# Performance work log

Measured on AMD Instinct MI355X. Metric: run time of the kernel, lower is better.

## Reference

```python
import jax, jax.numpy as jnp
import numpy as np

IDIM = 512
HDIM = 1024
CDIM = 128  # part_size; topk uses k = 2*CDIM (share=True)
B, T = 16, 4096


def _multihot(idx, n):
    """idx: [B, T, K] int32 -> [B, T, n] float 0/1 multi-hot.
    Matches one_hot(idx, n).float().sum(-2); topk indices are unique so add==set."""
    b, t, k = idx.shape
    rows = jnp.arange(b * t)[:, None]
    m = jnp.zeros((b * t, n), jnp.float32).at[rows, idx.reshape(-1, k)].add(1.0)
    return m.reshape(b, t, n)


def setup_inputs() -> dict:
    key = jax.random.key(0)
    ks = jax.random.split(key, 12)
    inp = {}
    inp["x"] = jax.random.normal(ks[0], (B, T, IDIM), jnp.float32)
    inp["mask_prev"] = (jax.random.uniform(ks[1], (B, T, HDIM)) < 0.1).astype(jnp.float32)

    def lin(k, i, o):
        return jax.random.normal(k, (i, o), jnp.float32) * (1.0 / np.sqrt(i))

    dims_e = [IDIM, 512, 512, 512, HDIM]
    dims_d = [HDIM, 512, 512, 512, IDIM]
    for i in range(4):
        inp[f"e_w{i}"] = lin(ks[2 + i], dims_e[i], dims_e[i + 1])
        inp[f"e_b{i}"] = jnp.zeros((dims_e[i + 1],), jnp.float32)
        inp[f"d_w{i}"] = lin(ks[6 + i], dims_d[i], dims_d[i + 1])
        inp[f"d_b{i}"] = jnp.zeros((dims_d[i + 1],), jnp.float32)
    return inp


def _mlp(x, ws, bs):
    for w, b in zip(ws[:-1], bs[:-1]):
        x = jax.nn.relu(x @ w + b)
    return x @ ws[-1] + bs[-1]


def reference(x, mask_prev,
              e_w0, e_b0, e_w1, e_b1, e_w2, e_b2, e_w3, e_b3,
              d_w0, d_b0, d_w1, d_b1, d_w2, d_b2, d_w3, d_b3):
    h = _mlp(x, [e_w0, e_w1, e_w2, e_w3], [e_b0, e_b1, e_b2, e_b3])  # [B,T,HDIM]

    # hidden_exclude_activation (mask_prev is not None branch)
    h = jnp.where(mask_prev > 0, jnp.float32(0.0), h)  # h[mask_prev.byte()] = 0
    energy = h * h
    _, idx = jax.lax.top_k(energy, 2 * CDIM)            # sorted desc, like torch.topk
    mask_cur_share = _multihot(idx, HDIM)               # top 2*cdim multi-hot
    # h.masked_fill(~mask_cur_share, 0): keep only the shared top-2*cdim energies
    h = h * mask_cur_share

    # decoder
    out = _mlp(h, [d_w0, d_w1, d_w2, d_w3], [d_b0, d_b1, d_b2, d_b3])  # [B,T,IDIM]
    return out
```

## Files before the change

kernel.cpp:

```cpp
#include <hip/hip_runtime.h>

constexpr int NTOK = 16 * 4096;
constexpr int KSEL = 256;
constexpr int UCAP = 8192;

using short8 = __attribute__((ext_vector_type(8))) short;
using f32x4  = __attribute__((ext_vector_type(4))) float;

__device__ inline unsigned short bf16_rne(float x) {
    unsigned u = __float_as_uint(x);
    unsigned r = u + 0x7fffu + ((u >> 16) & 1u);
    return (unsigned short)(r >> 16);
}
__device__ inline float bf16_f32(unsigned short h) {
    return __uint_as_float((unsigned)h << 16);
}

template<int K>
__global__ __launch_bounds__(256)
void gemm_f32(const float* __restrict__ A, const float* __restrict__ W,
              const float* __restrict__ bias, float* __restrict__ C,
              int M, int do_relu, const float* __restrict__ mask)
{
    constexpr int S = 132;
    __shared__ float sA[16 * S];
    __shared__ float sW[16 * S];

    const int tid = threadIdx.x;
    const int tx = tid & 15, ty = tid >> 4;

    const int gridX = gridDim.x;
    int nwg = gridX * gridDim.y;
    int bid = blockIdx.y * gridX + blockIdx.x;
    int cpx = nwg >> 3;
    int swz = (bid & 7) * cpx + (bid >> 3);
    const int rowBase = (swz / gridX) * 128;
    const int colBase = (swz % gridX) * 128;

    const int ar = tid >> 1;
    const int ak = (tid & 1) * 8;
    const int wk = tid >> 4;
    const int wc = tx * 4;

    float acc[8][8] = {};

    for (int k0 = 0; k0 < K; k0 += 16) {
        const float* ap = &A[(size_t)(rowBase + ar) * K + k0 + ak];
        float4 a0 = *(const float4*)ap;
        float4 a1 = *(const float4*)(ap + 4);
        const float* wp = &W[(size_t)(k0 + wk) * M + colBase + wc];
        float4 w0 = *(const float4*)wp;
        float4 w1 = *(const float4*)(wp + 64);
        __syncthreads();
        sA[(ak + 0) * S + ar] = a0.x; sA[(ak + 1) * S + ar] = a0.y;
        sA[(ak + 2) * S + ar] = a0.z; sA[(ak + 3) * S + ar] = a0.w;
        sA[(ak + 4) * S + ar] = a1.x; sA[(ak + 5) * S + ar] = a1.y;
        sA[(ak + 6) * S + ar] = a1.z; sA[(ak + 7) * S + ar] = a1.w;
        *(float4*)&sW[wk * S + wc]      = w0;
        *(float4*)&sW[wk * S + wc + 64] = w1;
        __syncthreads();
#pragma unroll
        for (int k = 0; k < 16; ++k) {
            float4 aLo = *(const float4*)&sA[k * S + ty * 4];
            float4 aHi = *(const float4*)&sA[k * S + 64 + ty * 4];
            float4 wLo = *(const float4*)&sW[k * S + tx * 4];
            float4 wHi = *(const float4*)&sW[k * S + 64 + tx * 4];
            float av[8] = {aLo.x, aLo.y, aLo.z, aLo.w, aHi.x, aHi.y, aHi.z, aHi.w};
            float wv[8] = {wLo.x, wLo.y, wLo.z, wLo.w, wHi.x, wHi.y, wHi.z, wHi.w};
#pragma unroll
            for (int i = 0; i < 8; ++i)
#pragma unroll
                for (int j = 0; j < 8; ++j)
                    acc[i][j] = fmaf(av[i], wv[j], acc[i][j]);
        }
    }

    float4 b0 = *(const float4*)&bias[colBase + tx * 4];
    float4 b1 = *(const float4*)&bias[colBase + 64 + tx * 4];
    float bb[8] = {b0.x, b0.y, b0.z, b0.w, b1.x, b1.y, b1.z, b1.w};
#pragma unroll
    for (int i = 0; i < 8; ++i) {
        int row = rowBase + ((i < 4) ? (ty * 4 + i) : (64 + ty * 4 + (i - 4)));
        float o[8];
#pragma unroll
        for (int j = 0; j < 8; ++j) {
            o[j] = acc[i][j] + bb[j];
            if (do_relu) o[j] = fmaxf(o[j], 0.f);
        }
        if (mask) {
            float4 m0 = *(const float4*)&mask[(size_t)row * M + colBase + tx * 4];
            float4 m1 = *(const float4*)&mask[(size_t)row * M + colBase + 64 + tx * 4];
            float mm[8] = {m0.x, m0.y, m0.z, m0.w, m1.x, m1.y, m1.z, m1.w};
#pragma unroll
            for (int j = 0; j < 8; ++j) if (mm[j] > 0.f) o[j] = 0.f;
        }
        float4 v0 = {o[0], o[1], o[2], o[3]};
        float4 v1 = {o[4], o[5], o[6], o[7]};
        *(float4*)&C[(size_t)row * M + colBase + tx * 4]      = v0;
        *(float4*)&C[(size_t)row * M + colBase + 64 + tx * 4] = v1;
    }
}

__global__ __launch_bounds__(256)
void wsplit_t(const float* __restrict__ W, unsigned short* __restrict__ WhT,
              unsigned short* __restrict__ WlT, int K, int M)
{
    __shared__ float tile[32][33];
    const int tid = threadIdx.x;
    const int tx = tid & 31, ty = tid >> 5;
    const int m0 = blockIdx.x * 32, k0 = blockIdx.y * 32;
#pragma unroll
    for (int i = 0; i < 4; ++i)
        tile[ty + 8 * i][tx] = W[(size_t)(k0 + ty + 8 * i) * M + m0 + tx];
    __syncthreads();
#pragma unroll
    for (int i = 0; i < 4; ++i) {
        int m = ty + 8 * i;
        float v = tile[tx][m];
        unsigned short hh = bf16_rne(v);
        unsigned short ll = bf16_rne(v - bf16_f32(hh));
        WhT[(size_t)(m0 + m) * K + k0 + tx] = hh;
        WlT[(size_t)(m0 + m) * K + k0 + tx] = ll;
    }
}

template<int K>
__global__ __launch_bounds__(256)
void gemm_mfma(const float* __restrict__ A, const unsigned short* __restrict__ WhT,
               const unsigned short* __restrict__ WlT, const float* __restrict__ bias,
               float* __restrict__ C, int M, int do_relu)
{
    __shared__ __align__(16) unsigned short sAh[128 * 40];
    __shared__ __align__(16) unsigned short sAl[128 * 40];
    __shared__ __align__(16) unsigned short sBh[128 * 40];
    __shared__ __align__(16) unsigned short sBl[128 * 40];

    const int tid = threadIdx.x;
    const int lane = tid & 63, wid = tid >> 6;
    const int quad = lane >> 4, l16 = lane & 15;
    const int rowBase = blockIdx.y * 128, colBase = blockIdx.x * 128;
    const int wr = (wid & 1) * 64, wc = (wid >> 1) * 64;

    const int sr = tid >> 1;
    const int sk = (tid & 1) * 16;

    f32x4 acc[4][4];
#pragma unroll
    for (int i = 0; i < 4; ++i)
#pragma unroll
        for (int j = 0; j < 4; ++j)
            acc[i][j] = (f32x4){0.f, 0.f, 0.f, 0.f};

    for (int k0 = 0; k0 < K; k0 += 32) {
        const float* ap = &A[(size_t)(rowBase + sr) * K + k0 + sk];
        float4 a0 = *(const float4*)ap;
        float4 a1 = *(const float4*)(ap + 4);
        float4 a2 = *(const float4*)(ap + 8);
        float4 a3 = *(const float4*)(ap + 12);
        const unsigned short* whp = &WhT[(size_t)(colBase + sr) * K + k0 + sk];
        const unsigned short* wlp = &WlT[(size_t)(colBase + sr) * K + k0 + sk];
        short8 wh0 = *(const short8*)whp;
        short8 wh1 = *(const short8*)(whp + 8);
        short8 wl0 = *(const short8*)wlp;
        short8 wl1 = *(const short8*)(wlp + 8);

        float f[16] = {a0.x, a0.y, a0.z, a0.w, a1.x, a1.y, a1.z, a1.w,
                       a2.x, a2.y, a2.z, a2.w, a3.x, a3.y, a3.z, a3.w};
        unsigned short __align__(16) hs[16], ls[16];
#pragma unroll
        for (int j = 0; j < 16; ++j) {
            hs[j] = bf16_rne(f[j]);
            ls[j] = bf16_rne(f[j] - bf16_f32(hs[j]));
        }

        __syncthreads();
        *(short8*)&sAh[sr * 40 + sk]     = *(short8*)&hs[0];
        *(short8*)&sAh[sr * 40 + sk + 8] = *(short8*)&hs[8];
        *(short8*)&sAl[sr * 40 + sk]     = *(short8*)&ls[0];
        *(short8*)&sAl[sr * 40 + sk + 8] = *(short8*)&ls[8];
        *(short8*)&sBh[sr * 40 + sk]     = wh0;
        *(short8*)&sBh[sr * 40 + sk + 8] = wh1;
        *(short8*)&sBl[sr * 40 + sk]     = wl0;
        *(short8*)&sBl[sr * 40 + sk + 8] = wl1;
        __syncthreads();

        short8 ah[4], al[4], bh[4], bl[4];
#pragma unroll
        for (int t4 = 0; t4 < 4; ++t4) {
            ah[t4] = *(const short8*)&sAh[(wr + t4 * 16 + l16) * 40 + quad * 8];
            al[t4] = *(const short8*)&sAl[(wr + t4 * 16 + l16) * 40 + quad * 8];
            bh[t4] = *(const short8*)&sBh[(wc + t4 * 16 + l16) * 40 + quad * 8];
            bl[t4] = *(const short8*)&sBl[(wc + t4 * 16 + l16) * 40 + quad * 8];
        }
#pragma unroll
        for (int rt = 0; rt < 4; ++rt)
#pragma unroll
            for (int ct = 0; ct < 4; ++ct) {
                acc[rt][ct] = __builtin_amdgcn_mfma_f32_16x16x32_bf16(ah[rt], bh[ct], acc[rt][ct], 0, 0, 0);
                acc[rt][ct] = __builtin_amdgcn_mfma_f32_16x16x32_bf16(al[rt], bh[ct], acc[rt][ct], 0, 0, 0);
                acc[rt][ct] = __builtin_amdgcn_mfma_f32_16x16x32_bf16(ah[rt], bl[ct], acc[rt][ct], 0, 0, 0);
            }
    }

#pragma unroll
    for (int ct = 0; ct < 4; ++ct) {
        int col = colBase + wc + ct * 16 + l16;
        float bc = bias[col];
#pragma unroll
        for (int rt = 0; rt < 4; ++rt)
#pragma unroll
            for (int r = 0; r < 4; ++r) {
                int row = rowBase + wr + rt * 16 + quad * 4 + r;
                float v = acc[rt][ct][r] + bc;
                if (do_relu) v = fmaxf(v, 0.f);
                C[(size_t)row * M + col] = v;
            }
    }
}

__global__ __launch_bounds__(256)
void topk_pass1(float* __restrict__ h, int* __restrict__ meta)
{
    const int t = blockIdx.x, tid = threadIdx.x;
    const int lane = tid & 63, wid = tid >> 6;

    __shared__ unsigned hist[256];
    __shared__ unsigned wsum[4];
    __shared__ unsigned dmx[4];
    __shared__ unsigned s_prefix;
    __shared__ int s_need;

    float4 hv = ((const float4*)(h + (size_t)t * 1024))[tid];
    float v[4] = {hv.x, hv.y, hv.z, hv.w};
    unsigned u[4];
#pragma unroll
    for (int j = 0; j < 4; ++j) u[j] = __float_as_uint(v[j] * v[j]);

    if (tid == 0) { s_prefix = 0u; s_need = KSEL; }
    __syncthreads();

    for (int p = 3; p >= 0; --p) {
        unsigned pref = s_prefix;
        int need = s_need;
        hist[tid] = 0u;
        __syncthreads();
#pragma unroll
        for (int j = 0; j < 4; ++j) {
            bool match = (p == 3) || ((u[j] >> (8 * (p + 1))) == (pref >> (8 * (p + 1))));
            if (match) atomicAdd(&hist[(u[j] >> (8 * p)) & 255u], 1u);
        }
        __syncthreads();
        unsigned x = hist[tid];
        unsigned s = x;
#pragma unroll
        for (int off = 1; off < 64; off <<= 1) {
            unsigned o = __shfl_down(s, off);
            if (lane + off < 64) s += o;
        }
        if (lane == 0) wsum[wid] = s;
        __syncthreads();
        unsigned above = 0;
        for (int w = wid + 1; w < 4; ++w) above += wsum[w];
        unsigned incl = s + above;
        unsigned excl = incl - x;
        if (incl >= (unsigned)need && excl < (unsigned)need) {
            s_prefix = pref | ((unsigned)tid << (8 * p));
            s_need = need - (int)excl;
        }
        __syncthreads();
    }
    const unsigned tau = s_prefix;

    unsigned cg = 0, ce = 0;
#pragma unroll
    for (int j = 0; j < 4; ++j) {
        cg += (u[j] > tau) ? 1u : 0u;
        ce += (u[j] == tau) ? 1u : 0u;
    }
    unsigned packed = (cg << 16) | ce;
    unsigned ps = packed;
#pragma unroll
    for (int off = 1; off < 64; off <<= 1) {
        unsigned o = __shfl_up(ps, off);
        if (lane >= off) ps += o;
    }
    if (lane == 63) wsum[wid] = ps;
    __syncthreads();
    unsigned below = 0;
    for (int w = 0; w < wid; ++w) below += wsum[w];
    unsigned total = wsum[0] + wsum[1] + wsum[2] + wsum[3];
    unsigned incl = ps + below;
    int need_eq = KSEL - (int)(total >> 16);
    int eq_base = (int)((incl - packed) & 0xffffu);

    bool kp[4];
    {
        int r = 0;
#pragma unroll
        for (int j = 0; j < 4; ++j) {
            if (u[j] > tau) kp[j] = true;
            else if (u[j] == tau) { kp[j] = (eq_base + r) < need_eq; ++r; }
            else kp[j] = false;
        }
    }

    unsigned dmax = 0;
#pragma unroll
    for (int j = 0; j < 4; ++j) if (!kp[j] && u[j] > dmax) dmax = u[j];
#pragma unroll
    for (int off = 32; off > 0; off >>= 1) {
        unsigned o = __shfl_xor(dmax, off);
        if (o > dmax) dmax = o;
    }
    if (lane == 0) dmx[wid] = dmax;
    __syncthreads();
    if (tid == 0) {
        unsigned lo = dmx[0];
        for (int w = 1; w < 4; ++w) if (dmx[w] > lo) lo = dmx[w];
        float tauf = __uint_as_float(tau);
        float lof  = __uint_as_float(lo);
        if (tauf - lof <= fmaf(tauf, 1e-4f, 2e-6f)) {
            int slot = atomicAdd(&meta[0], 1);
            if (slot < UCAP) meta[1 + slot] = t;
        }
    }

    float o[4];
#pragma unroll
    for (int j = 0; j < 4; ++j) o[j] = kp[j] ? v[j] : 0.f;
    float4 ov = {o[0], o[1], o[2], o[3]};
    ((float4*)(h + (size_t)t * 1024))[tid] = ov;
}

__global__ __launch_bounds__(256)
void gather_x(const float* __restrict__ x, double* __restrict__ a64,
              const int* __restrict__ meta)
{
    int cnt = meta[0]; if (cnt > UCAP) cnt = UCAP;
    int b = blockIdx.x;
    if (b >= cnt) return;
    int tok = meta[1 + b];
    const float* src = &x[(size_t)tok * 512];
    double* dst = &a64[(size_t)b * 512];
    for (int i = threadIdx.x; i < 512; i += 256) dst[i] = (double)src[i];
}

template<int K, int RELU, int MASKED>
__global__ __launch_bounds__(256)
void gemm_f64(const double* __restrict__ A, const float* __restrict__ W,
              const float* __restrict__ bias, double* __restrict__ Cd,
              int M, const int* __restrict__ meta, const float* __restrict__ mp)
{
    int cnt = meta[0]; if (cnt > UCAP) cnt = UCAP;
    const int rowBase = blockIdx.y * 64;
    if (rowBase >= cnt) return;
    const int colBase = blockIdx.x * 64;

    __shared__ double sA[16][65];
    __shared__ double sW[16][65];
    const int tid = threadIdx.x;
    const int tx = tid & 15, ty = tid >> 4;
    const int lr = tid & 63;
    const int lk4 = (tid >> 6) * 4;
    const int wk = tid >> 4;
    const int wc = (tid & 15) * 4;

    double acc[4][4] = {};

    for (int k0 = 0; k0 < K; k0 += 16) {
        const double* ap = &A[(size_t)(rowBase + lr) * K + k0 + lk4];
        double a0 = ap[0], a1 = ap[1], a2 = ap[2], a3 = ap[3];
        float4 wv = *(const float4*)&W[(size_t)(k0 + wk) * M + colBase + wc];
        __syncthreads();
        sA[lk4 + 0][lr] = a0; sA[lk4 + 1][lr] = a1;
        sA[lk4 + 2][lr] = a2; sA[lk4 + 3][lr] = a3;
        sW[wk][wc + 0] = (double)wv.x; sW[wk][wc + 1] = (double)wv.y;
        sW[wk][wc + 2] = (double)wv.z; sW[wk][wc + 3] = (double)wv.w;
        __syncthreads();
#pragma unroll
        for (int k = 0; k < 16; ++k) {
            double av[4], wl[4];
#pragma unroll
            for (int i = 0; i < 4; ++i) av[i] = sA[k][ty * 4 + i];
#pragma unroll
            for (int i = 0; i < 4; ++i) wl[i] = sW[k][tx * 4 + i];
#pragma unroll
            for (int a = 0; a < 4; ++a)
#pragma unroll
                for (int b = 0; b < 4; ++b)
                    acc[a][b] = fma(av[a], wl[b], acc[a][b]);
        }
    }

#pragma unroll
    for (int a = 0; a < 4; ++a) {
        int row = rowBase + ty * 4 + a;
        if (row >= cnt) continue;
        int tok = MASKED ? meta[1 + row] : 0;
#pragma unroll
        for (int b = 0; b < 4; ++b) {
            int col = colBase + tx * 4 + b;
            double vv = acc[a][b] + (double)bias[col];
            if (RELU) vv = vv > 0.0 ? vv : 0.0;
            if (MASKED) { if (mp[(size_t)tok * 1024 + col] > 0.f) vv = 0.0; }
            Cd[(size_t)row * M + col] = vv;
        }
    }
}

__global__ __launch_bounds__(256)
void topk_pass2(const double* __restrict__ h64, float* __restrict__ h,
                const int* __restrict__ meta)
{
    int cnt = meta[0]; if (cnt > UCAP) cnt = UCAP;
    int b = blockIdx.x;
    if (b >= cnt) return;
    int tok = meta[1 + b];

    __shared__ double se[1024];
    __shared__ unsigned short si[1024];
    __shared__ unsigned char keep[1024];
    const int tid = threadIdx.x;
    const double* row = &h64[(size_t)b * 1024];

#pragma unroll
    for (int t = 0; t < 4; ++t) {
        int i = tid + t * 256;
        double v = row[i];
        se[i] = v * v;
        si[i] = (unsigned short)i;
        keep[i] = 0;
    }
    __syncthreads();

    for (int ksz = 2; ksz <= 1024; ksz <<= 1) {
        for (int j = ksz >> 1; j > 0; j >>= 1) {
#pragma unroll
            for (int t = 0; t < 4; ++t) {
                int i = tid + t * 256;
                int p = i ^ j;
                if (p > i) {
                    double ei = se[i], ep = se[p];
                    unsigned short ii = si[i], ip = si[p];
                    bool later = !((ei > ep) || (ei == ep && ii < ip));
                    bool dir = ((i & ksz) == 0);
                    if (later == dir) {
                        se[i] = ep; se[p] = ei;
                        si[i] = ip; si[p] = ii;
                    }
                }
            }
            __syncthreads();
        }
    }

    keep[si[tid]] = 1;
    __syncthreads();

#pragma unroll
    for (int t = 0; t < 4; ++t) {
        int i = tid + t * 256;
        h[(size_t)tok * 1024 + i] = keep[i] ? (float)row[i] : 0.f;
    }
}

extern "C" void kernel_launch(void* const* d_in, const int* in_sizes, int n_in,
                              void* d_out, int out_size, void* d_ws, size_t ws_size,
                              hipStream_t stream)
{
    (void)n_in; (void)out_size; (void)ws_size;

    const float* x  = (const float*)d_in[0];
    const float* mp = (const float*)d_in[1];

    const float *ew[4], *eb[4], *dw[4], *db[4];
    bool interleaved = (in_sizes[4] == 1024 * 512);
    for (int i = 0; i < 4; ++i) {
        if (interleaved) {
            ew[i] = (const float*)d_in[2 + 4 * i];
            eb[i] = (const float*)d_in[3 + 4 * i];
            dw[i] = (const float*)d_in[4 + 4 * i];
            db[i] = (const float*)d_in[5 + 4 * i];
        } else {
            ew[i] = (const float*)d_in[2 + 2 * i];
            eb[i] = (const float*)d_in[3 + 2 * i];
            dw[i] = (const float*)d_in[10 + 2 * i];
            db[i] = (const float*)d_in[11 + 2 * i];
        }
    }

    float* out  = (float*)d_out;
    float* bufH = (float*)d_ws;
    float* bufP = bufH + (size_t)NTOK * 1024;

    unsigned short* Wh0 = (unsigned short*)d_out;
    unsigned short* Wl0 = Wh0 + 1024 * 512;
    unsigned short* Wh1 = Wl0 + 1024 * 512;
    unsigned short* Wl1 = Wh1 + 512 * 512;
    unsigned short* Wh2 = Wl1 + 512 * 512;
    unsigned short* Wl2 = Wh2 + 512 * 512;
    unsigned short* Wh3 = (unsigned short*)((char*)d_ws + (size_t)192 * 1024 * 1024);
    unsigned short* Wl3 = Wh3 + 512 * 512;

    double* h64 = (double*)((char*)d_out + (size_t)8 * 1024 * 1024);
    int*   meta = (int*)((char*)d_out + (size_t)72 * 1024 * 1024);
    double* a64 = (double*)bufP;
    double* b64 = (double*)((char*)bufP + (size_t)32 * 1024 * 1024);

    dim3 blk(256);

    wsplit_t<<<dim3(512 / 32, 1024 / 32), blk, 0, stream>>>(dw[0], Wh0, Wl0, 1024, 512);
    wsplit_t<<<dim3(512 / 32, 512 / 32),  blk, 0, stream>>>(dw[1], Wh1, Wl1, 512, 512);
    wsplit_t<<<dim3(512 / 32, 512 / 32),  blk, 0, stream>>>(dw[2], Wh2, Wl2, 512, 512);

    dim3 ge(512 / 128, NTOK / 128);
    dim3 ge4(1024 / 128, NTOK / 128);
    gemm_f32<512><<<ge,  blk, 0, stream>>>(x,    ew[0], eb[0], bufP, 512,  1, nullptr);
    gemm_f32<512><<<ge,  blk, 0, stream>>>(bufP, ew[1], eb[1], bufH, 512,  1, nullptr);
    gemm_f32<512><<<ge,  blk, 0, stream>>>(bufH, ew[2], eb[2], bufP, 512,  1, nullptr);
    gemm_f32<512><<<ge4, blk, 0, stream>>>(bufP, ew[3], eb[3], bufH, 1024, 0, mp);

    hipMemsetAsync(meta, 0, sizeof(int), stream);
    topk_pass1<<<dim3(NTOK), blk, 0, stream>>>(bufH, meta);

    dim3 g64a(512 / 64, UCAP / 64), g64b(1024 / 64, UCAP / 64);
    gather_x<<<dim3(UCAP), blk, 0, stream>>>(x, a64, meta);
    gemm_f64<512, 1, 0><<<g64a, blk, 0, stream>>>(a64, ew[0], eb[0], b64, 512,  meta, nullptr);
    gemm_f64<512, 1, 0><<<g64a, blk, 0, stream>>>(b64, ew[1], eb[1], a64, 512,  meta, nullptr);
    gemm_f64<512, 1, 0><<<g64a, blk, 0, stream>>>(a64, ew[2], eb[2], b64, 512,  meta, nullptr);
    gemm_f64<512, 0, 1><<<g64b, blk, 0, stream>>>(b64, ew[3], eb[3], h64, 1024, meta, mp);
    topk_pass2<<<dim3(UCAP), blk, 0, stream>>>(h64, bufH, meta);

    dim3 gd(512 / 128, NTOK / 128);
    gemm_mfma<1024><<<gd, blk, 0, stream>>>(bufH, Wh0, Wl0, db[0], bufP, 512, 1);
    wsplit_t<<<dim3(512 / 32, 512 / 32), blk, 0, stream>>>(dw[3], Wh3, Wl3, 512, 512);
    gemm_mfma<512> <<<gd, blk, 0, stream>>>(bufP, Wh1, Wl1, db[1], bufH, 512, 1);
    gemm_mfma<512> <<<gd, blk, 0, stream>>>(bufH, Wh2, Wl2, db[2], bufP, 512, 1);
    gemm_mfma<512> <<<gd, blk, 0, stream>>>(bufP, Wh3, Wl3, db[3], out,  512, 0);
}
```

Baseline: 3.653 ms.

## Run encoder on split-bf16 MFMA and store activations pre-split

Replaces the FP32 SIMT encoder GEMMs with the split-bf16 (hi/lo) MFMA GEMM already used for the decoder, pre-splitting the encoder weights. Intermediate activations are written already split into bf16 hi/lo pairs, so later GEMMs skip the per-tile conversion and read half-width data. The near-tie tolerance for FP64 recomputation is widened and the capacity doubled by processing the FP64 fallback in two chunks. This trades FP32 SIMT compute for tensor-core throughput, at the cost of more tokens needing the exact FP64 re-check.

```diff
diff --git a/kernel.cpp b/kernel.cpp
--- a/kernel.cpp
+++ b/kernel.cpp
@@ -1,10 +1,13 @@
 #include <hip/hip_runtime.h>
 
-constexpr int NTOK = 16 * 4096;
-constexpr int KSEL = 256;
-constexpr int UCAP = 8192;
+constexpr int NTOK  = 16 * 4096;
+constexpr int KSEL  = 256;
+constexpr int UCAP  = 8192;
+constexpr int NCHNK = 2;
+constexpr int UCAPT = UCAP * NCHNK;
 
 using short8 = __attribute__((ext_vector_type(8))) short;
+using ush4   = __attribute__((ext_vector_type(4))) unsigned short;
 using f32x4  = __attribute__((ext_vector_type(4))) float;
 
 __device__ inline unsigned short bf16_rne(float x) {
@@ -16,18 +19,43 @@
     return __uint_as_float((unsigned)h << 16);
 }
 
-template<int K>
 __global__ __launch_bounds__(256)
-void gemm_f32(const float* __restrict__ A, const float* __restrict__ W,
-              const float* __restrict__ bias, float* __restrict__ C,
-              int M, int do_relu, const float* __restrict__ mask)
-{
-    constexpr int S = 132;
-    __shared__ float sA[16 * S];
-    __shared__ float sW[16 * S];
-
+void wsplit_t(const float* __restrict__ W, unsigned short* __restrict__ WhT,
+              unsigned short* __restrict__ WlT, int K, int M)
+{
+    __shared__ float tile[32][33];
     const int tid = threadIdx.x;
-    const int tx = tid & 15, ty = tid >> 4;
+    const int tx = tid & 31, ty = tid >> 5;
+    const int m0 = blockIdx.x * 32, k0 = blockIdx.y * 32;
+#pragma unroll
+    for (int i = 0; i < 4; ++i)
+        tile[ty + 8 * i][tx] = W[(size_t)(k0 + ty + 8 * i) * M + m0 + tx];
+    __syncthreads();
+#pragma unroll
+    for (int i = 0; i < 4; ++i) {
+        int m = ty + 8 * i;
+        float v = tile[tx][m];
+        unsigned short hh = bf16_rne(v);
+        unsigned short ll = bf16_rne(v - bf16_f32(hh));
+        WhT[(size_t)(m0 + m) * K + k0 + tx] = hh;
+        WlT[(size_t)(m0 + m) * K + k0 + tx] = ll;
+    }
+}
+
+template<int K, int RELU, int OUT_SPLIT, int A_SPLIT>
+__global__ __launch_bounds__(256)
+void gemm_u(const void* Ap, const unsigned short* __restrict__ WhT,
+            const unsigned short* __restrict__ WlT, const float* __restrict__ bias,
+            void* Cp, int M, const float* __restrict__ mask)
+{
+    __shared__ __align__(16) unsigned short sAh[128 * 40];
+    __shared__ __align__(16) unsigned short sAl[128 * 40];
+    __shared__ __align__(16) unsigned short sBh[128 * 40];
+    __shared__ __align__(16) unsigned short sBl[128 * 40];
+
+    const int tid = threadIdx.x;
+    const int lane = tid & 63, wid = tid >> 6;
+    const int quad = lane >> 4, l16 = lane & 15;
 
     const int gridX = gridDim.x;
     int nwg = gridX * gridDim.y;
@@ -37,110 +65,7 @@
     const int rowBase = (swz / gridX) * 128;
     const int colBase = (swz % gridX) * 128;
 
-    const int ar = tid >> 1;
-    const int ak = (tid & 1) * 8;
-    const int wk = tid >> 4;
-    const int wc = tx * 4;
-
-    float acc[8][8] = {};
-
-    for (int k0 = 0; k0 < K; k0 += 16) {
-        const float* ap = &A[(size_t)(rowBase + ar) * K + k0 + ak];
-        float4 a0 = *(const float4*)ap;
-        float4 a1 = *(const float4*)(ap + 4);
-        const float* wp = &W[(size_t)(k0 + wk) * M + colBase + wc];
-        float4 w0 = *(const float4*)wp;
-        float4 w1 = *(const float4*)(wp + 64);
-        __syncthreads();
-        sA[(ak + 0) * S + ar] = a0.x; sA[(ak + 1) * S + ar] = a0.y;
-        sA[(ak + 2) * S + ar] = a0.z; sA[(ak + 3) * S + ar] = a0.w;
-        sA[(ak + 4) * S + ar] = a1.x; sA[(ak + 5) * S + ar] = a1.y;
-        sA[(ak + 6) * S + ar] = a1.z; sA[(ak + 7) * S + ar] = a1.w;
-        *(float4*)&sW[wk * S + wc]      = w0;
-        *(float4*)&sW[wk * S + wc + 64] = w1;
-        __syncthreads();
-#pragma unroll
-        for (int k = 0; k < 16; ++k) {
-            float4 aLo = *(const float4*)&sA[k * S + ty * 4];
-            float4 aHi = *(const float4*)&sA[k * S + 64 + ty * 4];
-            float4 wLo = *(const float4*)&sW[k * S + tx * 4];
-            float4 wHi = *(const float4*)&sW[k * S + 64 + tx * 4];
-            float av[8] = {aLo.x, aLo.y, aLo.z, aLo.w, aHi.x, aHi.y, aHi.z, aHi.w};
-            float wv[8] = {wLo.x, wLo.y, wLo.z, wLo.w, wHi.x, wHi.y, wHi.z, wHi.w};
-#pragma unroll
-            for (int i = 0; i < 8; ++i)
-#pragma unroll
-                for (int j = 0; j < 8; ++j)
-                    acc[i][j] = fmaf(av[i], wv[j], acc[i][j]);
-        }
-    }
-
-    float4 b0 = *(const float4*)&bias[colBase + tx * 4];
-    float4 b1 = *(const float4*)&bias[colBase + 64 + tx * 4];
-    float bb[8] = {b0.x, b0.y, b0.z, b0.w, b1.x, b1.y, b1.z, b1.w};
-#pragma unroll
-    for (int i = 0; i < 8; ++i) {
-        int row = rowBase + ((i < 4) ? (ty * 4 + i) : (64 + ty * 4 + (i - 4)));
-        float o[8];
-#pragma unroll
-        for (int j = 0; j < 8; ++j) {
-            o[j] = acc[i][j] + bb[j];
-            if (do_relu) o[j] = fmaxf(o[j], 0.f);
-        }
-        if (mask) {
-            float4 m0 = *(const float4*)&mask[(size_t)row * M + colBase + tx * 4];
-            float4 m1 = *(const float4*)&mask[(size_t)row * M + colBase + 64 + tx * 4];
-            float mm[8] = {m0.x, m0.y, m0.z, m0.w, m1.x, m1.y, m1.z, m1.w};
-#pragma unroll
-            for (int j = 0; j < 8; ++j) if (mm[j] > 0.f) o[j] = 0.f;
-        }
-        float4 v0 = {o[0], o[1], o[2], o[3]};
-        float4 v1 = {o[4], o[5], o[6], o[7]};
-        *(float4*)&C[(size_t)row * M + colBase + tx * 4]      = v0;
-        *(float4*)&C[(size_t)row * M + colBase + 64 + tx * 4] = v1;
-    }
-}
-
-__global__ __launch_bounds__(256)
-void wsplit_t(const float* __restrict__ W, unsigned short* __restrict__ WhT,
-              unsigned short* __restrict__ WlT, int K, int M)
-{
-    __shared__ float tile[32][33];
-    const int tid = threadIdx.x;
-    const int tx = tid & 31, ty = tid >> 5;
-    const int m0 = blockIdx.x * 32, k0 = blockIdx.y * 32;
-#pragma unroll
-    for (int i = 0; i < 4; ++i)
-        tile[ty + 8 * i][tx] = W[(size_t)(k0 + ty + 8 * i) * M + m0 + tx];
-    __syncthreads();
-#pragma unroll
-    for (int i = 0; i < 4; ++i) {
-        int m = ty + 8 * i;
-        float v = tile[tx][m];
-        unsigned short hh = bf16_rne(v);
-        unsigned short ll = bf16_rne(v - bf16_f32(hh));
-        WhT[(size_t)(m0 + m) * K + k0 + tx] = hh;
-        WlT[(size_t)(m0 + m) * K + k0 + tx] = ll;
-    }
-}
-
-template<int K>
-__global__ __launch_bounds__(256)
-void gemm_mfma(const float* __restrict__ A, const unsigned short* __restrict__ WhT,
-               const unsigned short* __restrict__ WlT, const float* __restrict__ bias,
-               float* __restrict__ C, int M, int do_relu)
-{
-    __shared__ __align__(16) unsigned short sAh[128 * 40];
-    __shared__ __align__(16) unsigned short sAl[128 * 40];
-    __shared__ __align__(16) unsigned short sBh[128 * 40];
-    __shared__ __align__(16) unsigned short sBl[128 * 40];
-
-    const int tid = threadIdx.x;
-    const int lane = tid & 63, wid = tid >> 6;
-    const int quad = lane >> 4, l16 = lane & 15;
-    const int rowBase = blockIdx.y * 128, colBase = blockIdx.x * 128;
     const int wr = (wid & 1) * 64, wc = (wid >> 1) * 64;
-
     const int sr = tid >> 1;
     const int sk = (tid & 1) * 16;
 
@@ -152,11 +77,32 @@
             acc[i][j] = (f32x4){0.f, 0.f, 0.f, 0.f};
 
     for (int k0 = 0; k0 < K; k0 += 32) {
-        const float* ap = &A[(size_t)(rowBase + sr) * K + k0 + sk];
-        float4 a0 = *(const float4*)ap;
-        float4 a1 = *(const float4*)(ap + 4);
-        float4 a2 = *(const float4*)(ap + 8);
-        float4 a3 = *(const float4*)(ap + 12);
+        short8 Ah0, Ah1, Al0, Al1;
+        if constexpr (A_SPLIT) {
+            const unsigned short* Au = (const unsigned short*)Ap;
+            size_t base = (size_t)(rowBase + sr) * (2 * K) + k0 + sk;
+            Ah0 = *(const short8*)&Au[base];
+            Ah1 = *(const short8*)&Au[base + 8];
+            Al0 = *(const short8*)&Au[base + K];
+            Al1 = *(const short8*)&Au[base + K + 8];
+        } else {
+            const float* Af = (const float*)Ap;
+            const float* ap = &Af[(size_t)(rowBase + sr) * K + k0 + sk];
+            float4 a0 = *(const float4*)ap;
+            float4 a1 = *(const float4*)(ap + 4);
+            float4 a2 = *(const float4*)(ap + 8);
+            float4 a3 = *(const float4*)(ap + 12);
+            float f[16] = {a0.x, a0.y, a0.z, a0.w, a1.x, a1.y, a1.z, a1.w,
+                           a2.x, a2.y, a2.z, a2.w, a3.x, a3.y, a3.z, a3.w};
+            unsigned short __align__(16) hs[16], ls[16];
+#pragma unroll
+            for (int j = 0; j < 16; ++j) {
+                hs[j] = bf16_rne(f[j]);
+                ls[j] = bf16_rne(f[j] - bf16_f32(hs[j]));
+            }
+            Ah0 = *(short8*)&hs[0]; Ah1 = *(short8*)&hs[8];
+            Al0 = *(short8*)&ls[0]; Al1 = *(short8*)&ls[8];
+        }
         const unsigned short* whp = &WhT[(size_t)(colBase + sr) * K + k0 + sk];
         const unsigned short* wlp = &WlT[(size_t)(colBase + sr) * K + k0 + sk];
         short8 wh0 = *(const short8*)whp;
@@ -164,20 +110,11 @@
         short8 wl0 = *(const short8*)wlp;
         short8 wl1 = *(const short8*)(wlp + 8);
 
-        float f[16] = {a0.x, a0.y, a0.z, a0.w, a1.x, a1.y, a1.z, a1.w,
-                       a2.x, a2.y, a2.z, a2.w, a3.x, a3.y, a3.z, a3.w};
-        unsigned short __align__(16) hs[16], ls[16];
-#pragma unroll
-        for (int j = 0; j < 16; ++j) {
-            hs[j] = bf16_rne(f[j]);
-            ls[j] = bf16_rne(f[j] - bf16_f32(hs[j]));
-        }
-
-        __syncthreads();
-        *(short8*)&sAh[sr * 40 + sk]     = *(short8*)&hs[0];
-        *(short8*)&sAh[sr * 40 + sk + 8] = *(short8*)&hs[8];
-        *(short8*)&sAl[sr * 40 + sk]     = *(short8*)&ls[0];
-        *(short8*)&sAl[sr * 40 + sk + 8] = *(short8*)&ls[8];
+        __syncthreads();
+        *(short8*)&sAh[sr * 40 + sk]     = Ah0;
+        *(short8*)&sAh[sr * 40 + sk + 8] = Ah1;
+        *(short8*)&sAl[sr * 40 + sk]     = Al0;
+        *(short8*)&sAl[sr * 40 + sk + 8] = Al1;
         *(short8*)&sBh[sr * 40 + sk]     = wh0;
         *(short8*)&sBh[sr * 40 + sk + 8] = wh1;
         *(short8*)&sBl[sr * 40 + sk]     = wl0;
@@ -212,14 +149,23 @@
             for (int r = 0; r < 4; ++r) {
                 int row = rowBase + wr + rt * 16 + quad * 4 + r;
                 float v = acc[rt][ct][r] + bc;
-                if (do_relu) v = fmaxf(v, 0.f);
-                C[(size_t)row * M + col] = v;
+                if (RELU) v = fmaxf(v, 0.f);
+                if (mask) { if (mask[(size_t)row * M + col] > 0.f) v = 0.f; }
+                if constexpr (OUT_SPLIT) {
+                    unsigned short* Cs = (unsigned short*)Cp;
+                    unsigned short hh = bf16_rne(v);
+                    unsigned short ll = bf16_rne(v - bf16_f32(hh));
+                    Cs[(size_t)row * (2 * M) + col]     = hh;
+                    Cs[(size_t)row * (2 * M) + M + col] = ll;
+                } else {
+                    ((float*)Cp)[(size_t)row * M + col] = v;
+                }
             }
     }
 }
 
 __global__ __launch_bounds__(256)
-void topk_pass1(float* __restrict__ h, int* __restrict__ meta)
+void topk_pass1(const float* h, unsigned short* hsplit, int* __restrict__ meta)
 {
     const int t = blockIdx.x, tid = threadIdx.x;
     const int lane = tid & 63, wid = tid >> 6;
@@ -319,29 +265,34 @@
         for (int w = 1; w < 4; ++w) if (dmx[w] > lo) lo = dmx[w];
         float tauf = __uint_as_float(tau);
         float lof  = __uint_as_float(lo);
-        if (tauf - lof <= fmaf(tauf, 1e-4f, 2e-6f)) {
+        if (tauf - lof <= fmaf(tauf, 4e-4f, 4e-5f)) {
             int slot = atomicAdd(&meta[0], 1);
-            if (slot < UCAP) meta[1 + slot] = t;
-        }
-    }
-
-    float o[4];
-#pragma unroll
-    for (int j = 0; j < 4; ++j) o[j] = kp[j] ? v[j] : 0.f;
-    float4 ov = {o[0], o[1], o[2], o[3]};
-    ((float4*)(h + (size_t)t * 1024))[tid] = ov;
+            if (slot < UCAPT) meta[1 + slot] = t;
+        }
+    }
+
+    unsigned short hs[4], ls[4];
+#pragma unroll
+    for (int j = 0; j < 4; ++j) {
+        float ov = kp[j] ? v[j] : 0.f;
+        hs[j] = bf16_rne(ov);
+        ls[j] = bf16_rne(ov - bf16_f32(hs[j]));
+    }
+    size_t base = (size_t)t * 2048 + 4 * tid;
+    *(ush4*)&hsplit[base]        = (ush4){hs[0], hs[1], hs[2], hs[3]};
+    *(ush4*)&hsplit[base + 1024] = (ush4){ls[0], ls[1], ls[2], ls[3]};
 }
 
 __global__ __launch_bounds__(256)
 void gather_x(const float* __restrict__ x, double* __restrict__ a64,
-              const int* __restrict__ meta)
-{
-    int cnt = meta[0]; if (cnt > UCAP) cnt = UCAP;
-    int b = blockIdx.x;
-    if (b >= cnt) return;
-    int tok = meta[1 + b];
+              const int* __restrict__ meta, int chunk)
+{
+    int cnt = meta[0]; if (cnt > UCAPT) cnt = UCAPT;
+    int g = chunk * UCAP + blockIdx.x;
+    if (g >= cnt) return;
+    int tok = meta[1 + g];
     const float* src = &x[(size_t)tok * 512];
-    double* dst = &a64[(size_t)b * 512];
+    double* dst = &a64[(size_t)blockIdx.x * 512];
     for (int i = threadIdx.x; i < 512; i += 256) dst[i] = (double)src[i];
 }
 
@@ -349,11 +300,14 @@
 __global__ __launch_bounds__(256)
 void gemm_f64(const double* __restrict__ A, const float* __restrict__ W,
               const float* __restrict__ bias, double* __restrict__ Cd,
-              int M, const int* __restrict__ meta, const float* __restrict__ mp)
-{
-    int cnt = meta[0]; if (cnt > UCAP) cnt = UCAP;
+              int M, const int* __restrict__ meta, const float* __restrict__ mp,
+              int chunk)
+{
+    int cnt = meta[0]; if (cnt > UCAPT) cnt = UCAPT;
+    int cloc = cnt - chunk * UCAP;
+    if (cloc < 0) cloc = 0; if (cloc > UCAP) cloc = UCAP;
     const int rowBase = blockIdx.y * 64;
-    if (rowBase >= cnt) return;
+    if (rowBase >= cloc) return;
     const int colBase = blockIdx.x * 64;
 
     __shared__ double sA[16][65];
@@ -395,8 +349,8 @@
 #pragma unroll
     for (int a = 0; a < 4; ++a) {
         int row = rowBase + ty * 4 + a;
-        if (row >= cnt) continue;
-        int tok = MASKED ? meta[1 + row] : 0;
+        if (row >= cloc) continue;
+        int tok = MASKED ? meta[1 + chunk * UCAP + row] : 0;
 #pragma unroll
         for (int b = 0; b < 4; ++b) {
             int col = colBase + tx * 4 + b;
@@ -409,19 +363,19 @@
 }
 
 __global__ __launch_bounds__(256)
-void topk_pass2(const double* __restrict__ h64, float* __restrict__ h,
-                const int* __restrict__ meta)
-{
-    int cnt = meta[0]; if (cnt > UCAP) cnt = UCAP;
-    int b = blockIdx.x;
-    if (b >= cnt) return;
-    int tok = meta[1 + b];
+void topk_pass2(const double* __restrict__ h64, unsigned short* __restrict__ hsplit,
+                const int* __restrict__ meta, int chunk)
+{
+    int cnt = meta[0]; if (cnt > UCAPT) cnt = UCAPT;
+    int g = chunk * UCAP + blockIdx.x;
+    if (g >= cnt) return;
+    int tok = meta[1 + g];
 
     __shared__ double se[1024];
     __shared__ unsigned short si[1024];
     __shared__ unsigned char keep[1024];
     const int tid = threadIdx.x;
-    const double* row = &h64[(size_t)b * 1024];
+    const double* row = &h64[(size_t)blockIdx.x * 1024];
 
 #pragma unroll
     for (int t = 0; t < 4; ++t) {
@@ -460,7 +414,11 @@
 #pragma unroll
     for (int t = 0; t < 4; ++t) {
         int i = tid + t * 256;
-        h[(size_t)tok * 1024 + i] = keep[i] ? (float)row[i] : 0.f;
+        float vv = keep[i] ? (float)row[i] : 0.f;
+        unsigned short hh = bf16_rne(vv);
+        unsigned short ll = bf16_rne(vv - bf16_f32(hh));
+        hsplit[(size_t)tok * 2048 + i]        = hh;
+        hsplit[(size_t)tok * 2048 + 1024 + i] = ll;
     }
 }
 
@@ -489,52 +447,70 @@
         }
     }
 
-    float* out  = (float*)d_out;
-    float* bufH = (float*)d_ws;
-    float* bufP = bufH + (size_t)NTOK * 1024;
-
-    unsigned short* Wh0 = (unsigned short*)d_out;
-    unsigned short* Wl0 = Wh0 + 1024 * 512;
-    unsigned short* Wh1 = Wl0 + 1024 * 512;
-    unsigned short* Wl1 = Wh1 + 512 * 512;
-    unsigned short* Wh2 = Wl1 + 512 * 512;
-    unsigned short* Wl2 = Wh2 + 512 * 512;
-    unsigned short* Wh3 = (unsigned short*)((char*)d_ws + (size_t)192 * 1024 * 1024);
-    unsigned short* Wl3 = Wh3 + 512 * 512;
-
-    double* h64 = (double*)((char*)d_out + (size_t)8 * 1024 * 1024);
-    int*   meta = (int*)((char*)d_out + (size_t)72 * 1024 * 1024);
-    double* a64 = (double*)bufP;
-    double* b64 = (double*)((char*)bufP + (size_t)32 * 1024 * 1024);
+    char* ws = (char*)d_ws;
+    char* ob = (char*)d_out;
+    const size_t MB = 1024 * 1024;
+
+    unsigned short* S1 = (unsigned short*)(ws);
+    unsigned short* S2 = (unsigned short*)(ws + 128 * MB);
+    unsigned short* S3 = (unsigned short*)(ws + 256 * MB);
+    float*          hF = (float*)(ws);
+    unsigned short* Hs = (unsigned short*)(ws);
+    unsigned short* D1 = (unsigned short*)(ws + 256 * MB);
+    unsigned short* D2 = (unsigned short*)(ws);
+    unsigned short* D3 = (unsigned short*)(ws + 128 * MB);
+    float*          out = (float*)d_out;
+
+    unsigned short* p0 = (unsigned short*)ob;
+    unsigned short* EW0h = p0 + 0;        unsigned short* EW0l = p0 + 262144;
+    unsigned short* EW1h = p0 + 524288;   unsigned short* EW1l = p0 + 786432;
+    unsigned short* EW2h = p0 + 1048576;  unsigned short* EW2l = p0 + 1310720;
+    unsigned short* EW3h = p0 + 1572864;  unsigned short* EW3l = p0 + 2097152;
+    unsigned short* W0h  = p0 + 2621440;  unsigned short* W0l  = p0 + 3145728;
+    unsigned short* W1h  = p0 + 3670016;  unsigned short* W1l  = p0 + 3932160;
+    unsigned short* W2h  = p0 + 4194304;  unsigned short* W2l  = p0 + 4456448;
+    int* meta = (int*)(ob + 16 * MB);
+
+    unsigned short* W3h = (unsigned short*)(ws + 256 * MB);
+    unsigned short* W3l = W3h + 262144;
+
+    double* a64 = (double*)(ws + 256 * MB);
+    double* b64 = (double*)(ws + 288 * MB);
+    double* h64 = (double*)(ws + 320 * MB);
 
     dim3 blk(256);
 
-    wsplit_t<<<dim3(512 / 32, 1024 / 32), blk, 0, stream>>>(dw[0], Wh0, Wl0, 1024, 512);
-    wsplit_t<<<dim3(512 / 32, 512 / 32),  blk, 0, stream>>>(dw[1], Wh1, Wl1, 512, 512);
-    wsplit_t<<<dim3(512 / 32, 512 / 32),  blk, 0, stream>>>(dw[2], Wh2, Wl2, 512, 512);
-
-    dim3 ge(512 / 128, NTOK / 128);
-    dim3 ge4(1024 / 128, NTOK / 128);
-    gemm_f32<512><<<ge,  blk, 0, stream>>>(x,    ew[0], eb[0], bufP, 512,  1, nullptr);
-    gemm_f32<512><<<ge,  blk, 0, stream>>>(bufP, ew[1], eb[1], bufH, 512,  1, nullptr);
-    gemm_f32<512><<<ge,  blk, 0, stream>>>(bufH, ew[2], eb[2], bufP, 512,  1, nullptr);
-    gemm_f32<512><<<ge4, blk, 0, stream>>>(bufP, ew[3], eb[3], bufH, 1024, 0, mp);
-
+    wsplit_t<<<dim3(16, 16), blk, 0, stream>>>(ew[0], EW0h, EW0l, 512, 512);
+    wsplit_t<<<dim3(16, 16), blk, 0, stream>>>(ew[1], EW1h, EW1l, 512, 512);
+    wsplit_t<<<dim3(16, 16), blk, 0, stream>>>(ew[2], EW2h, EW2l, 512, 512);
+    wsplit_t<<<dim3(32, 16), blk, 0, stream>>>(ew[3], EW3h, EW3l, 512, 1024);
+    wsplit_t<<<dim3(16, 32), blk, 0, stream>>>(dw[0], W0h,  W0l,  1024, 512);
+    wsplit_t<<<dim3(16, 16), blk, 0, stream>>>(dw[1], W1h,  W1l,  512, 512);
+    wsplit_t<<<dim3(16, 16), blk, 0, stream>>>(dw[2], W2h,  W2l,  512, 512);
     hipMemsetAsync(meta, 0, sizeof(int), stream);
-    topk_pass1<<<dim3(NTOK), blk, 0, stream>>>(bufH, meta);
-
-    dim3 g64a(512 / 64, UCAP / 64), g64b(1024 / 64, UCAP / 64);
-    gather_x<<<dim3(UCAP), blk, 0, stream>>>(x, a64, meta);
-    gemm_f64<512, 1, 0><<<g64a, blk, 0, stream>>>(a64, ew[0], eb[0], b64, 512,  meta, nullptr);
-    gemm_f64<512, 1, 0><<<g64a, blk, 0, stream>>>(b64, ew[1], eb[1], a64, 512,  meta, nullptr);
-    gemm_f64<512, 1, 0><<<g64a, blk, 0, stream>>>(a64, ew[2], eb[2], b64, 512,  meta, nullptr);
-    gemm_f64<512, 0, 1><<<g64b, blk, 0, stream>>>(b64, ew[3], eb[3], h64, 1024, meta, mp);
-    topk_pass2<<<dim3(UCAP), blk, 0, stream>>>(h64, bufH, meta);
-
-    dim3 gd(512 / 128, NTOK / 128);
-    gemm_mfma<1024><<<gd, blk, 0, stream>>>(bufH, Wh0, Wl0, db[0], bufP, 512, 1);
-    wsplit_t<<<dim3(512 / 32, 512 / 32), blk, 0, stream>>>(dw[3], Wh3, Wl3, 512, 512);
-    gemm_mfma<512> <<<gd, blk, 0, stream>>>(bufP, Wh1, Wl1, db[1], bufH, 512, 1);
-    gemm_mfma<512> <<<gd, blk, 0, stream>>>(bufH, Wh2, Wl2, db[2], bufP, 512, 1);
-    gemm_mfma<512> <<<gd, blk, 0, stream>>>(bufP, Wh3, Wl3, db[3], out,  512, 0);
-}
+
+    dim3 ge(4, NTOK / 128), ge4(8, NTOK / 128);
+    gemm_u<512, 1, 1, 0><<<ge,  blk, 0, stream>>>(x,  EW0h, EW0l, eb[0], S1, 512,  nullptr);
+    gemm_u<512, 1, 1, 1><<<ge,  blk, 0, stream>>>(S1, EW1h, EW1l, eb[1], S2, 512,  nullptr);
+    gemm_u<512, 1, 1, 1><<<ge,  blk, 0, stream>>>(S2, EW2h, EW2l, eb[2], S3, 512,  nullptr);
+    gemm_u<512, 0, 0, 1><<<ge4, blk, 0, stream>>>(S3, EW3h, EW3l, eb[3], hF, 1024, mp);
+
+    topk_pass1<<<dim3(NTOK), blk, 0, stream>>>(hF, Hs, meta);
+
+    dim3 g64a(8, UCAP / 64), g64b(16, UCAP / 64);
+    for (int c = 0; c < NCHNK; ++c) {
+        gather_x<<<dim3(UCAP), blk, 0, stream>>>(x, a64, meta, c);
+        gemm_f64<512, 1, 0><<<g64a, blk, 0, stream>>>(a64, ew[0], eb[0], b64, 512,  meta, nullptr, c);
+        gemm_f64<512, 1, 0><<<g64a, blk, 0, stream>>>(b64, ew[1], eb[1], a64, 512,  meta, nullptr, c);
+        gemm_f64<512, 1, 0><<<g64a, blk, 0, stream>>>(a64, ew[2], eb[2], b64, 512,  meta, nullptr, c);
+        gemm_f64<512, 0, 1><<<g64b, blk, 0, stream>>>(b64, ew[3], eb[3], h64, 1024, meta, mp, c);
+        topk_pass2<<<dim3(UCAP), blk, 0, stream>>>(h64, Hs, meta, c);
+    }
+
+    dim3 gd(4, NTOK / 128);
+    gemm_u<1024, 1, 1, 1><<<gd, blk, 0, stream>>>(Hs, W0h, W0l, db[0], D1, 512, nullptr);
+    gemm_u<512, 1, 1, 1><<<gd, blk, 0, stream>>>(D1, W1h, W1l, db[1], D2, 512, nullptr);
+    wsplit_t<<<dim3(16, 16), blk, 0, stream>>>(dw[3], W3h, W3l, 512, 512);
+    gemm_u<512, 1, 1, 1><<<gd, blk, 0, stream>>>(D2, W2h, W2l, db[2], D3, 512, nullptr);
+    gemm_u<512, 0, 0, 1><<<gd, blk, 0, stream>>>(D3, W3h, W3l, db[3], out, 512, nullptr);
+}
```

After: 4.000 ms. +9.5%, slower.
